# Performance work log

Measured on AMD Instinct MI355X. Metric: run time of the kernel, lower is better.

The kernel has to match this reference:

```python
import jax, jax.numpy as jnp
import numpy as np

EPS = 1e-8


def setup_inputs() -> dict:
    key = jax.random.key(0)
    k1, k2, k3 = jax.random.split(key, 3)
    B, N, M, C = 4, 4096, 16384, 256
    xyz = jax.random.normal(k1, (B * N, 3), dtype=jnp.float32)
    new_xyz = jax.random.normal(k2, (B * M, 3), dtype=jnp.float32)
    feat = jax.random.normal(k3, (B * N, C), dtype=jnp.float32)
    offset = jnp.arange(1, B + 1, dtype=jnp.int64) * N      # [4096, 8192, 12288, 16384]
    new_offset = jnp.arange(1, B + 1, dtype=jnp.int64) * M  # [16384, ..., 65536]
    return {"xyz": xyz, "new_xyz": new_xyz, "feat": feat,
            "offset": offset, "new_offset": new_offset, "k": 3}


def _interpolate(xyz_b, new_xyz_b, feat_b, k):
    # xyz_b: [B,N,3], new_xyz_b: [B,M,3], feat_b: [B,N,C]
    # pairwise squared distances via GEMM: [B,M,N]
    q2 = jnp.sum(new_xyz_b * new_xyz_b, axis=-1, keepdims=True)        # [B,M,1]
    s2 = jnp.sum(xyz_b * xyz_b, axis=-1)[:, None, :]                   # [B,1,N]
    cross = jnp.einsum('bmd,bnd->bmn', new_xyz_b, xyz_b)               # [B,M,N]
    d2 = q2 + s2 - 2.0 * cross                                         # [B,M,N]
    neg_d2, idx = jax.lax.top_k(-d2, k)                                # [B,M,k]
    dist = jnp.sqrt(jnp.maximum(-neg_d2, 1e-12))                       # euclidean, like knnquery
    dist_recip = 1.0 / (dist + EPS)
    weight = dist_recip / jnp.sum(dist_recip, axis=-1, keepdims=True)  # [B,M,k]
    gathered = jax.vmap(lambda f, i: f[i])(feat_b, idx)                # [B,M,k,C]
    return jnp.einsum('bmkc,bmk->bmc', gathered, weight)               # [B,M,C]


def reference(xyz, new_xyz, feat, offset, new_offset, k):
    B = offset.shape[0]
    N = xyz.shape[0] // B
    M = new_xyz.shape[0] // B
    C = feat.shape[1]
    # uniform offsets -> reshape into per-cloud batches
    out = _interpolate(xyz.reshape(B, N, 3), new_xyz.reshape(B, M, 3),
                       feat.reshape(B, N, C), k)
    return out.reshape(B * M, C)
```

## Files before the change

### kernel.cpp

```cpp
#include <hip/hip_runtime.h>
#include <float.h>


#define QPL   2
#define QPB   128
#define SPLIT 8
#define KEY_INIT 0x7FEFFFFFFFFFFFFFULL

#define NCA   16
#define NC    (NCA * NCA * NCA)
#define GMIN  (-4.0f)
#define HCELL (0.5f)
#define INVH  (2.0f)
#define SLACK (1e-3f)

typedef float v2f __attribute__((ext_vector_type(2)));

__device__ __forceinline__ double mk_key(float d2, int j) {
    unsigned long long u =
        ((unsigned long long)(unsigned)__float_as_uint(d2) << 32) | (unsigned)j;
    return __longlong_as_double(u);
}

__device__ __forceinline__ void ins3(double key, double& k0, double& k1,
                                     double& k2) {
    const double n0 = fmin(key, k0);
    const double n1 = fmin(fmax(key, k0), k1);
    const double n2 = fmin(fmax(key, k1), k2);
    k0 = n0; k1 = n1; k2 = n2;
}

__device__ __forceinline__ v2f dist2_pair(const v2f qx2, const v2f qy2,
                                          const v2f qz2, const v2f q22,
                                          const float4 p) {
    #pragma clang fp contract(off)
    const v2f px = {p.x, p.x};
    const v2f py = {p.y, p.y};
    const v2f pz = {p.z, p.z};
    const v2f pw = {p.w, p.w};
    const v2f t0 = qx2 * px;
    const v2f t1 = qy2 * py;
    const v2f t2 = t0 + t1;
    const v2f t3 = qz2 * pz;
    const v2f cr = t2 + t3;
    const v2f qs = q22 + pw;
    const v2f cc = cr + cr;
    const v2f d2 = qs - cc;
    return d2;
}

__device__ __forceinline__ float dist2_scalar(float qx, float qy, float qz,
                                              float q2, const float4 p) {
    #pragma clang fp contract(off)
    const float t0 = qx * p.x;
    const float t1 = qy * p.y;
    const float t2 = t0 + t1;
    const float t3 = qz * p.z;
    const float cr = t2 + t3;
    const float qs = q2 + p.w;
    const float cc = cr + cr;
    const float d2 = qs - cc;
    return d2;
}

__device__ __forceinline__ float sum_sq3(float x, float y, float z) {
    return __fadd_rn(__fadd_rn(__fmul_rn(x, x), __fmul_rn(y, y)),
                     __fmul_rn(z, z));
}

__device__ __forceinline__ int clampi(int v, int lo, int hi) {
    return v < lo ? lo : (v > hi ? hi : v);
}

__device__ __forceinline__ void cell3(float x, float y, float z,
                                      int& cx, int& cy, int& cz) {
    cx = clampi((int)floorf((x - GMIN) * INVH), 0, NCA - 1);
    cy = clampi((int)floorf((y - GMIN) * INVH), 0, NCA - 1);
    cz = clampi((int)floorf((z - GMIN) * INVH), 0, NCA - 1);
}

__global__ __launch_bounds__(1024) void grid_build(
    const float* __restrict__ xyz, const float* __restrict__ new_xyz,
    int* __restrict__ start, int* __restrict__ qstart,
    float4* __restrict__ spts, int* __restrict__ sidx,
    int* __restrict__ qsrt, int N, int M, int B)
{
    __shared__ int hist[NC];
    __shared__ int psum[1024];

    const int blk = blockIdx.x;
    const bool isQ = blk >= B;
    const int b = isQ ? blk - B : blk;
    const int nItems = isQ ? M : N;
    const float* __restrict__ src = isQ ? new_xyz + (size_t)b * M * 3
                                        : xyz + (size_t)b * N * 3;
    int* __restrict__ dst = isQ ? qstart : start;
    const int base = isQ ? b * M : b * N;
    const int t = threadIdx.x;

    #pragma unroll
    for (int c = t; c < NC; c += 1024) hist[c] = 0;
    __syncthreads();

    for (int i = t; i < nItems; i += 1024) {
        int cx, cy, cz;
        cell3(src[(size_t)i * 3 + 0], src[(size_t)i * 3 + 1],
              src[(size_t)i * 3 + 2], cx, cy, cz);
        atomicAdd(&hist[(cz * NCA + cy) * NCA + cx], 1);
    }
    __syncthreads();

    int loc0 = hist[t * 4 + 0], loc1 = hist[t * 4 + 1];
    int loc2 = hist[t * 4 + 2], loc3 = hist[t * 4 + 3];
    psum[t] = loc0 + loc1 + loc2 + loc3;
    __syncthreads();
    for (int off = 1; off < 1024; off <<= 1) {
        int v = 0;
        if (t >= off) v = psum[t - off];
        __syncthreads();
        psum[t] += v;
        __syncthreads();
    }
    int run = (t == 0 ? 0 : psum[t - 1]);
    dst[b * NC + t * 4 + 0] = base + run;  hist[t * 4 + 0] = run;  run += loc0;
    dst[b * NC + t * 4 + 1] = base + run;  hist[t * 4 + 1] = run;  run += loc1;
    dst[b * NC + t * 4 + 2] = base + run;  hist[t * 4 + 2] = run;  run += loc2;
    dst[b * NC + t * 4 + 3] = base + run;  hist[t * 4 + 3] = run;  run += loc3;
    if (!isQ && b == B - 1 && t == 1023) start[B * NC] = B * N;
    __syncthreads();

    for (int i = t; i < nItems; i += 1024) {
        const float x = src[(size_t)i * 3 + 0];
        const float y = src[(size_t)i * 3 + 1];
        const float z = src[(size_t)i * 3 + 2];
        int cx, cy, cz;
        cell3(x, y, z, cx, cy, cz);
        const int c = (cz * NCA + cy) * NCA + cx;
        const int slot = base + atomicAdd(&hist[c], 1);
        if (isQ) {
            qsrt[slot] = b * M + i;
        } else {
            spts[slot] = make_float4(x, y, z, sum_sq3(x, y, z));
            sidx[slot] = i;
        }
    }
}

__global__ __launch_bounds__(256, 8) void fp_knn_gather(
    const float* __restrict__ new_xyz,
    const float4* __restrict__ spts, const int* __restrict__ sidx,
    const int* __restrict__ start, const int* __restrict__ qsrt,
    const float4* __restrict__ feat4, float4* __restrict__ out4,
    int N, int M, int B) {
    __shared__ int   s_jb[16][3];
    __shared__ float s_wb[16][3];
    __shared__ int   s_qid[16];

    const int tid = threadIdx.x;
    const int grp = tid >> 4;
    const int s   = tid & 15;
    const int p   = blockIdx.x * 16 + grp;
    const int qid = qsrt[p];
    const int b   = qid / M;
    const int bNC = b * NC;

    const float qx = new_xyz[(size_t)qid * 3 + 0];
    const float qy = new_xyz[(size_t)qid * 3 + 1];
    const float qz = new_xyz[(size_t)qid * 3 + 2];
    const float q2 = sum_sq3(qx, qy, qz);

    int cx, cy, cz;
    cell3(qx, qy, qz, cx, cy, cz);

    const float bx0 = GMIN + (float)cx * HCELL;
    const float by0 = GMIN + (float)cy * HCELL;
    const float bz0 = GMIN + (float)cz * HCELL;
    const float ex = fmaxf(fmaxf(bx0 - qx, qx - (bx0 + HCELL)), 0.0f);
    const float ey = fmaxf(fmaxf(by0 - qy, qy - (by0 + HCELL)), 0.0f);
    const float ez = fmaxf(fmaxf(bz0 - qz, qz - (bz0 + HCELL)), 0.0f);
    const float e = fmaxf(ex, fmaxf(ey, ez));

    double k0 = __longlong_as_double(KEY_INIT), k1 = k0, k2 = k0;

    auto seg = [&](int x0, int x1, int cy2, int cz2) {
        const int rowbase = bNC + (cz2 * NCA + cy2) * NCA;
        const int j0 = start[rowbase + x0];
        const int j1 = start[rowbase + x1 + 1];
        for (int j = j0 + s; j < j1; j += 16) {
            const float4 pt = spts[j];
            const float d2 = dist2_scalar(qx, qy, qz, q2, pt);
            ins3(mk_key(d2, sidx[j]), k0, k1, k2);
        }
    };

    auto merge16 = [&](double& o0, double& o1, double& o2) {
        double t0 = k0, t1 = k1, t2 = k2;
        #pragma unroll
        for (int mask = 1; mask <= 8; mask <<= 1) {
            const double r0 = __shfl_xor(t0, mask, 16);
            const double r1 = __shfl_xor(t1, mask, 16);
            const double r2 = __shfl_xor(t2, mask, 16);
            ins3(r0, t0, t1, t2);
            ins3(r1, t0, t1, t2);
            ins3(r2, t0, t1, t2);
        }
        o0 = t0; o1 = t1; o2 = t2;
    };

    {
        const int z0 = clampi(cz - 1, 0, NCA - 1), z1 = clampi(cz + 1, 0, NCA - 1);
        const int y0 = clampi(cy - 1, 0, NCA - 1), y1 = clampi(cy + 1, 0, NCA - 1);
        const int x0 = clampi(cx - 1, 0, NCA - 1), x1 = clampi(cx + 1, 0, NCA - 1);
        for (int cz2 = z0; cz2 <= z1; ++cz2)
            for (int cy2 = y0; cy2 <= y1; ++cy2)
                seg(x0, x1, cy2, cz2);
    }

    for (int r = 2; r < NCA; ++r) {
        double m0, m1, m2;
        merge16(m0, m1, m2);
        const float d3 = __uint_as_float(
            (unsigned)((unsigned long long)__double_as_longlong(m2) >> 32));
        const float lb = fmaxf(HCELL * (float)(r - 1) - e, 0.0f);
        if (lb * lb > d3 + SLACK) break;
        const int z0 = clampi(cz - r, 0, NCA - 1), z1 = clampi(cz + r, 0, NCA - 1);
        const int y0 = clampi(cy - r, 0, NCA - 1), y1 = clampi(cy + r, 0, NCA - 1);
        const int x0 = clampi(cx - r, 0, NCA - 1), x1 = clampi(cx + r, 0, NCA - 1);
        for (int cz2 = z0; cz2 <= z1; ++cz2) {
            const int adz = cz2 >= cz ? cz2 - cz : cz - cz2;
            for (int cy2 = y0; cy2 <= y1; ++cy2) {
                const int ady = cy2 >= cy ? cy2 - cy : cy - cy2;
                if (adz == r || ady == r) {
                    seg(x0, x1, cy2, cz2);
                } else {
                    if (cx - r >= 0)       seg(cx - r, cx - r, cy2, cz2);
                    if (cx + r <= NCA - 1) seg(cx + r, cx + r, cy2, cz2);
                }
            }
        }
    }

    double f0, f1, f2;
    merge16(f0, f1, f2);
    if (s == 0) {
        const unsigned long long u0 = __double_as_longlong(f0);
        const unsigned long long u1 = __double_as_longlong(f1);
        const unsigned long long u2 = __double_as_longlong(f2);
        const float d0 = __uint_as_float((unsigned)(u0 >> 32));
        const float d1 = __uint_as_float((unsigned)(u1 >> 32));
        const float d2f = __uint_as_float((unsigned)(u2 >> 32));
        const float e0 = sqrtf(fmaxf(d0, 1e-12f));
        const float e1 = sqrtf(fmaxf(d1, 1e-12f));
        const float e2 = sqrtf(fmaxf(d2f, 1e-12f));
        const float r0 = 1.0f / (e0 + 1e-8f);
        const float r1 = 1.0f / (e1 + 1e-8f);
        const float r2 = 1.0f / (e2 + 1e-8f);
        const float rs = r0 + r1 + r2;
        s_jb[grp][0] = (int)(u0 & 0xffffffffu);
        s_jb[grp][1] = (int)(u1 & 0xffffffffu);
        s_jb[grp][2] = (int)(u2 & 0xffffffffu);
        s_wb[grp][0] = r0 / rs; s_wb[grp][1] = r1 / rs; s_wb[grp][2] = r2 / rs;
        s_qid[grp] = qid;
    }
    __syncthreads();

    const int lane = tid & 63;
    const int wv   = tid >> 6;
    #pragma unroll
    for (int t = 0; t < 4; ++t) {
        const int qq = wv * 4 + t;
        const int qid2 = s_qid[qq];
        const int b2 = qid2 / M;
        const int src_base = b2 * N;
        const int   a0 = s_jb[qq][0], a1 = s_jb[qq][1], a2 = s_jb[qq][2];
        const float u0 = s_wb[qq][0], u1 = s_wb[qq][1], u2 = s_wb[qq][2];
        const float4 f0v = feat4[(size_t)(src_base + a0) * 64 + lane];
        const float4 f1v = feat4[(size_t)(src_base + a1) * 64 + lane];
        const float4 f2v = feat4[(size_t)(src_base + a2) * 64 + lane];
        float4 o;
        o.x = u0 * f0v.x + u1 * f1v.x + u2 * f2v.x;
        o.y = u0 * f0v.y + u1 * f1v.y + u2 * f2v.y;
        o.z = u0 * f0v.z + u1 * f1v.z + u2 * f2v.z;
        o.w = u0 * f0v.w + u1 * f1v.w + u2 * f2v.w;
        out4[(size_t)qid2 * 64 + lane] = o;
    }
}

__global__ void pack_pts(const float* __restrict__ xyz,
                         float4* __restrict__ pts, int total) {
    int i = blockIdx.x * blockDim.x + threadIdx.x;
    if (i < total) {
        const float sx = xyz[(size_t)i * 3 + 0];
        const float sy = xyz[(size_t)i * 3 + 1];
        const float sz = xyz[(size_t)i * 3 + 2];
        pts[i] = make_float4(sx, sy, sz, sum_sq3(sx, sy, sz));
    }
}

template <int CHUNK>
__global__ __launch_bounds__(512, 4) void fp_knn_main(
    const float* __restrict__ new_xyz, const float4* __restrict__ pts,
    const float4* __restrict__ feat4, float4* __restrict__ out4,
    int N, int blocks_per_batch) {
    __shared__ double s_k[SPLIT][QPB][3];
    __shared__ float  s_w[QPB][3];
    __shared__ int    s_j[QPB][3];

    int g = blockIdx.x;
    if (gridDim.x == 512 && blocks_per_batch == 128) {
        const int xcd = g & 7, slot = g >> 3;
        g = (xcd >> 1) * 128 + (xcd & 1) * 64 + slot;
    }

    const int tid  = threadIdx.x;
    const int lane = tid & 63;
    const int b    = g / blocks_per_batch;
    const int src_base = b * N;
    const int m0 = g * QPB + lane;
    const int m1 = m0 + 64;

    const float q0x = new_xyz[(size_t)m0 * 3 + 0];
    const float q0y = new_xyz[(size_t)m0 * 3 + 1];
    const float q0z = new_xyz[(size_t)m0 * 3 + 2];
    const float q1x = new_xyz[(size_t)m1 * 3 + 0];
    const float q1y = new_xyz[(size_t)m1 * 3 + 1];
    const float q1z = new_xyz[(size_t)m1 * 3 + 2];
    const v2f qx2 = {q0x, q1x};
    const v2f qy2 = {q0y, q1y};
    const v2f qz2 = {q0z, q1z};
    const v2f q22 = {sum_sq3(q0x, q0y, q0z), sum_sq3(q1x, q1y, q1z)};

    const int cw    = tid >> 6;
    const int cbase = cw * CHUNK;
    const float4* __restrict__ cp = pts + src_base + cbase;

    double k00 = __longlong_as_double(KEY_INIT);
    double k01 = k00, k02 = k00;
    double k10 = k00, k11 = k00, k12 = k00;

    #pragma unroll 8
    for (int j = 0; j < CHUNK; ++j) {
        const float4 p = cp[j];
        const v2f d2 = dist2_pair(qx2, qy2, qz2, q22, p);
        ins3(mk_key(d2.x, cbase + j), k00, k01, k02);
        ins3(mk_key(d2.y, cbase + j), k10, k11, k12);
    }

    s_k[cw][lane][0]      = k00; s_k[cw][lane][1]      = k01; s_k[cw][lane][2]      = k02;
    s_k[cw][lane + 64][0] = k10; s_k[cw][lane + 64][1] = k11; s_k[cw][lane + 64][2] = k12;
    __syncthreads();

    if (tid < QPB) {
        double m0k = __longlong_as_double(KEY_INIT), m1k = m0k, m2k = m0k;
        #pragma unroll
        for (int ss = 0; ss < SPLIT; ++ss) {
            #pragma unroll
            for (int r = 0; r < 3; ++r) ins3(s_k[ss][tid][r], m0k, m1k, m2k);
        }
        unsigned long long u0 = __double_as_longlong(m0k);
        unsigned long long u1 = __double_as_longlong(m1k);
        unsigned long long u2 = __double_as_longlong(m2k);
        const float d0 = __uint_as_float((unsigned)(u0 >> 32));
        const float d1 = __uint_as_float((unsigned)(u1 >> 32));
        const float d2 = __uint_as_float((unsigned)(u2 >> 32));
        const float e0 = sqrtf(fmaxf(d0, 1e-12f));
        const float e1 = sqrtf(fmaxf(d1, 1e-12f));
        const float e2 = sqrtf(fmaxf(d2, 1e-12f));
        const float r0 = 1.0f / (e0 + 1e-8f);
        const float r1 = 1.0f / (e1 + 1e-8f);
        const float r2 = 1.0f / (e2 + 1e-8f);
        const float rs = r0 + r1 + r2;
        s_w[tid][0] = r0 / rs; s_w[tid][1] = r1 / rs; s_w[tid][2] = r2 / rs;
        s_j[tid][0] = (int)(u0 & 0xffffffffu);
        s_j[tid][1] = (int)(u1 & 0xffffffffu);
        s_j[tid][2] = (int)(u2 & 0xffffffffu);
    }
    __syncthreads();

    const int wv    = tid >> 6;
    const int qbase = g * QPB;
    #pragma unroll 4
    for (int t = 0; t < QPB / SPLIT; ++t) {
        const int qq = wv * (QPB / SPLIT) + t;
        const int   a0 = s_j[qq][0], a1 = s_j[qq][1], a2 = s_j[qq][2];
        const float u0 = s_w[qq][0], u1 = s_w[qq][1], u2 = s_w[qq][2];
        const float4 f0 = feat4[(size_t)(src_base + a0) * 64 + lane];
        const float4 f1 = feat4[(size_t)(src_base + a1) * 64 + lane];
        const float4 f2 = feat4[(size_t)(src_base + a2) * 64 + lane];
        float4 o;
        o.x = u0 * f0.x + u1 * f1.x + u2 * f2.x;
        o.y = u0 * f0.y + u1 * f1.y + u2 * f2.y;
        o.z = u0 * f0.z + u1 * f1.z + u2 * f2.z;
        o.w = u0 * f0.w + u1 * f1.w + u2 * f2.w;
        out4[(size_t)(qbase + qq) * 64 + lane] = o;
    }
}

__global__ void fp_knn_generic(
    const float* __restrict__ new_xyz, const float* __restrict__ xyz,
    const float* __restrict__ feat, float* __restrict__ out,
    int N, int M, int Btot) {
    const int m = blockIdx.x * blockDim.x + threadIdx.x;
    if (m >= Btot * M) return;
    const int b = m / M;
    const int src_base = b * N;
    const float qx = new_xyz[(size_t)m * 3 + 0];
    const float qy = new_xyz[(size_t)m * 3 + 1];
    const float qz = new_xyz[(size_t)m * 3 + 2];
    const float q2 = sum_sq3(qx, qy, qz);
    double k0 = __longlong_as_double(KEY_INIT), k1 = k0, k2 = k0;
    for (int j = 0; j < N; ++j) {
        const float sx = xyz[(size_t)(src_base + j) * 3 + 0];
        const float sy = xyz[(size_t)(src_base + j) * 3 + 1];
        const float sz = xyz[(size_t)(src_base + j) * 3 + 2];
        const float4 p = make_float4(sx, sy, sz, sum_sq3(sx, sy, sz));
        const float d2 = dist2_scalar(qx, qy, qz, q2, p);
        ins3(mk_key(d2, j), k0, k1, k2);
    }
    unsigned long long u0 = __double_as_longlong(k0);
    unsigned long long u1 = __double_as_longlong(k1);
    unsigned long long u2 = __double_as_longlong(k2);
    const float e0 = sqrtf(fmaxf(__uint_as_float((unsigned)(u0 >> 32)), 1e-12f));
    const float e1 = sqrtf(fmaxf(__uint_as_float((unsigned)(u1 >> 32)), 1e-12f));
    const float e2 = sqrtf(fmaxf(__uint_as_float((unsigned)(u2 >> 32)), 1e-12f));
    const float r0 = 1.0f / (e0 + 1e-8f);
    const float r1 = 1.0f / (e1 + 1e-8f);
    const float r2 = 1.0f / (e2 + 1e-8f);
    const float rs = r0 + r1 + r2;
    const float w0 = r0 / rs, w1 = r1 / rs, w2 = r2 / rs;
    const int a0 = (int)(u0 & 0xffffffffu), a1 = (int)(u1 & 0xffffffffu),
              a2 = (int)(u2 & 0xffffffffu);
    const int C = 256;
    for (int c = 0; c < C; ++c) {
        out[(size_t)m * C + c] =
            w0 * feat[(size_t)(src_base + a0) * C + c] +
            w1 * feat[(size_t)(src_base + a1) * C + c] +
            w2 * feat[(size_t)(src_base + a2) * C + c];
    }
}

extern "C" void kernel_launch(void* const* d_in, const int* in_sizes, int n_in,
                              void* d_out, int out_size, void* d_ws, size_t ws_size,
                              hipStream_t stream) {
    const float* xyz     = (const float*)d_in[0];
    const float* new_xyz = (const float*)d_in[1];
    const float* feat    = (const float*)d_in[2];
    float* out = (float*)d_out;

    const int B = in_sizes[3];
    const int N = in_sizes[0] / (3 * B);
    const int M = in_sizes[1] / (3 * B);
    const int Q = B * M;

    auto al = [](size_t x) { return (x + 255) & ~(size_t)255; };
    const size_t o_spts   = 0;
    const size_t o_sidx   = o_spts  + al((size_t)B * N * 16);
    const size_t o_start  = o_sidx  + al((size_t)B * N * 4);
    const size_t o_qstart = o_start + al(((size_t)B * NC + 1) * 4);
    const size_t o_qsort  = o_qstart+ al((size_t)B * NC * 4);
    const size_t need_grid = o_qsort + al((size_t)Q * 4);

    if ((Q % 16 == 0) && ws_size >= need_grid) {
        char* w = (char*)d_ws;
        float4* spts  = (float4*)(w + o_spts);
        int*   sidx   = (int*)  (w + o_sidx);
        int*   start  = (int*)  (w + o_start);
        int*   qstart = (int*)  (w + o_qstart);
        int*   qsrt   = (int*)  (w + o_qsort);

        grid_build<<<2 * B, 1024, 0, stream>>>(
            xyz, new_xyz, start, qstart, spts, sidx, qsrt, N, M, B);
        fp_knn_gather<<<Q / 16, 256, 0, stream>>>(
            new_xyz, spts, sidx, start, qsrt, (const float4*)feat,
            (float4*)out, N, M, B);
        return;
    }

    const size_t pts_bytes = (size_t)(B * N) * sizeof(float4);
    const bool fused_ok = (N % SPLIT == 0) && (N / SPLIT == 512) &&
                          (M % QPB == 0) && (ws_size >= pts_bytes);
    if (fused_ok) {
        pack_pts<<<(B * N + 255) / 256, 256, 0, stream>>>(xyz, (float4*)d_ws, B * N);
        const int blocks = Q / QPB;
        fp_knn_main<512><<<blocks, 512, 0, stream>>>(
            new_xyz, (const float4*)d_ws, (const float4*)feat, (float4*)out,
            N, M / QPB);
    } else {
        fp_knn_generic<<<(Q + 255) / 256, 256, 0, stream>>>(
            new_xyz, xyz, feat, out, N, M, B);
    }
}
```

Baseline: 199.7 us.

## Prune neighbor cells by box distance and gather per group without shared memory

The first ring of 26 neighbor cells is no longer scanned unconditionally. The kernel scans the query's own cell first, then visits each neighbor only if its box lower-bound distance is within the current group's third-nearest distance, refreshing that bound after each cell with a float-only shuffle merge. The final gather is done directly by each 16-lane group from registers, which removes the shared-memory staging and __syncthreads. The occupancy hint is also lowered. In exchange, there are more shuffle merges and per-cell start lookups, and the gather issues narrower 16-lane accesses per row.

```diff
diff --git a/kernel.cpp b/kernel.cpp
--- a/kernel.cpp
+++ b/kernel.cpp
@@ -28,6 +28,20 @@
     const double n1 = fmin(fmax(key, k0), k1);
     const double n2 = fmin(fmax(key, k1), k2);
     k0 = n0; k1 = n1; k2 = n2;
+}
+
+__device__ __forceinline__ void ins3f(float v, float& v0, float& v1,
+                                      float& v2) {
+    const float n0 = fminf(v, v0);
+    const float n1 = fminf(fmaxf(v, v0), v1);
+    const float n2 = fminf(fmaxf(v, v1), v2);
+    v0 = n0; v1 = n1; v2 = n2;
+}
+
+__device__ __forceinline__ float key_d2(double k) {
+    const unsigned long long u = __double_as_longlong(k);
+    const float v = __uint_as_float((unsigned)(u >> 32));
+    return (v == v) ? v : FLT_MAX;
 }
 
 __device__ __forceinline__ v2f dist2_pair(const v2f qx2, const v2f qy2,
@@ -146,16 +160,12 @@
     }
 }
 
-__global__ __launch_bounds__(256, 8) void fp_knn_gather(
+__global__ __launch_bounds__(256, 4) void fp_knn_gather(
     const float* __restrict__ new_xyz,
     const float4* __restrict__ spts, const int* __restrict__ sidx,
     const int* __restrict__ start, const int* __restrict__ qsrt,
     const float4* __restrict__ feat4, float4* __restrict__ out4,
     int N, int M, int B) {
-    __shared__ int   s_jb[16][3];
-    __shared__ float s_wb[16][3];
-    __shared__ int   s_qid[16];
-
     const int tid = threadIdx.x;
     const int grp = tid >> 4;
     const int s   = tid & 15;
@@ -175,6 +185,17 @@
     const float bx0 = GMIN + (float)cx * HCELL;
     const float by0 = GMIN + (float)cy * HCELL;
     const float bz0 = GMIN + (float)cz * HCELL;
+
+    const float dxm = fmaxf(0.0f, fmaxf((bx0 - HCELL) - qx, qx - bx0));
+    const float dxp = fmaxf(0.0f, fmaxf((bx0 + HCELL) - qx, qx - (bx0 + 2.0f * HCELL)));
+    const float dym = fmaxf(0.0f, fmaxf((by0 - HCELL) - qy, qy - by0));
+    const float dyp = fmaxf(0.0f, fmaxf((by0 + HCELL) - qy, qy - (by0 + 2.0f * HCELL)));
+    const float dzm = fmaxf(0.0f, fmaxf((bz0 - HCELL) - qz, qz - bz0));
+    const float dzp = fmaxf(0.0f, fmaxf((bz0 + HCELL) - qz, qz - (bz0 + 2.0f * HCELL)));
+    const float sqx[3] = {dxm * dxm, 0.0f, dxp * dxp};
+    const float sqy[3] = {dym * dym, 0.0f, dyp * dyp};
+    const float sqz[3] = {dzm * dzm, 0.0f, dzp * dzp};
+
     const float ex = fmaxf(fmaxf(bx0 - qx, qx - (bx0 + HCELL)), 0.0f);
     const float ey = fmaxf(fmaxf(by0 - qy, qy - (by0 + HCELL)), 0.0f);
     const float ez = fmaxf(fmaxf(bz0 - qz, qz - (bz0 + HCELL)), 0.0f);
@@ -182,7 +203,18 @@
 
     double k0 = __longlong_as_double(KEY_INIT), k1 = k0, k2 = k0;
 
-    auto seg = [&](int x0, int x1, int cy2, int cz2) {
+    auto scan_cell = [&](int cellIdx) {
+        const int gidx = bNC + cellIdx;
+        const int j0 = start[gidx];
+        const int j1 = start[gidx + 1];
+        for (int j = j0 + s; j < j1; j += 16) {
+            const float4 pt = spts[j];
+            const float d2 = dist2_scalar(qx, qy, qz, q2, pt);
+            ins3(mk_key(d2, sidx[j]), k0, k1, k2);
+        }
+    };
+
+    auto scan_span = [&](int x0, int x1, int cy2, int cz2) {
         const int rowbase = bNC + (cz2 * NCA + cy2) * NCA;
         const int j0 = start[rowbase + x0];
         const int j1 = start[rowbase + x1 + 1];
@@ -193,36 +225,47 @@
         }
     };
 
-    auto merge16 = [&](double& o0, double& o1, double& o2) {
-        double t0 = k0, t1 = k1, t2 = k2;
+    auto group_d3 = [&]() -> float {
+        float v0 = key_d2(k0), v1 = key_d2(k1), v2 = key_d2(k2);
         #pragma unroll
         for (int mask = 1; mask <= 8; mask <<= 1) {
-            const double r0 = __shfl_xor(t0, mask, 16);
-            const double r1 = __shfl_xor(t1, mask, 16);
-            const double r2 = __shfl_xor(t2, mask, 16);
-            ins3(r0, t0, t1, t2);
-            ins3(r1, t0, t1, t2);
-            ins3(r2, t0, t1, t2);
-        }
-        o0 = t0; o1 = t1; o2 = t2;
+            const float r0 = __shfl_xor(v0, mask, 16);
+            const float r1 = __shfl_xor(v1, mask, 16);
+            const float r2 = __shfl_xor(v2, mask, 16);
+            ins3f(r0, v0, v1, v2);
+            ins3f(r1, v0, v1, v2);
+            ins3f(r2, v0, v1, v2);
+        }
+        return v2;
     };
 
+    scan_cell((cz * NCA + cy) * NCA + cx);
+    float d3g = group_d3();
+
     {
-        const int z0 = clampi(cz - 1, 0, NCA - 1), z1 = clampi(cz + 1, 0, NCA - 1);
-        const int y0 = clampi(cy - 1, 0, NCA - 1), y1 = clampi(cy + 1, 0, NCA - 1);
-        const int x0 = clampi(cx - 1, 0, NCA - 1), x1 = clampi(cx + 1, 0, NCA - 1);
-        for (int cz2 = z0; cz2 <= z1; ++cz2)
-            for (int cy2 = y0; cy2 <= y1; ++cy2)
-                seg(x0, x1, cy2, cz2);
+        static constexpr int off[26][3] = {
+            {-1,0,0},{1,0,0},{0,-1,0},{0,1,0},{0,0,-1},{0,0,1},
+            {-1,-1,0},{-1,1,0},{1,-1,0},{1,1,0},
+            {-1,0,-1},{-1,0,1},{1,0,-1},{1,0,1},
+            {0,-1,-1},{0,-1,1},{0,1,-1},{0,1,1},
+            {-1,-1,-1},{-1,-1,1},{-1,1,-1},{-1,1,1},
+            {1,-1,-1},{1,-1,1},{1,1,-1},{1,1,1}};
+        #pragma unroll
+        for (int n = 0; n < 26; ++n) {
+            const int ox = off[n][0], oy = off[n][1], oz = off[n][2];
+            const int nx = cx + ox, ny = cy + oy, nz = cz + oz;
+            if (nx < 0 || nx >= NCA || ny < 0 || ny >= NCA ||
+                nz < 0 || nz >= NCA) continue;
+            const float db2 = sqx[ox + 1] + sqy[oy + 1] + sqz[oz + 1];
+            if (db2 > d3g + SLACK) continue;
+            scan_cell((nz * NCA + ny) * NCA + nx);
+            d3g = group_d3();
+        }
     }
 
     for (int r = 2; r < NCA; ++r) {
-        double m0, m1, m2;
-        merge16(m0, m1, m2);
-        const float d3 = __uint_as_float(
-            (unsigned)((unsigned long long)__double_as_longlong(m2) >> 32));
         const float lb = fmaxf(HCELL * (float)(r - 1) - e, 0.0f);
-        if (lb * lb > d3 + SLACK) break;
+        if (lb * lb > d3g + SLACK) break;
         const int z0 = clampi(cz - r, 0, NCA - 1), z1 = clampi(cz + r, 0, NCA - 1);
         const int y0 = clampi(cy - r, 0, NCA - 1), y1 = clampi(cy + r, 0, NCA - 1);
         const int x0 = clampi(cx - r, 0, NCA - 1), x1 = clampi(cx + r, 0, NCA - 1);
@@ -231,58 +274,62 @@
             for (int cy2 = y0; cy2 <= y1; ++cy2) {
                 const int ady = cy2 >= cy ? cy2 - cy : cy - cy2;
                 if (adz == r || ady == r) {
-                    seg(x0, x1, cy2, cz2);
+                    scan_span(x0, x1, cy2, cz2);
                 } else {
-                    if (cx - r >= 0)       seg(cx - r, cx - r, cy2, cz2);
-                    if (cx + r <= NCA - 1) seg(cx + r, cx + r, cy2, cz2);
+                    if (cx - r >= 0)       scan_span(cx - r, cx - r, cy2, cz2);
+                    if (cx + r <= NCA - 1) scan_span(cx + r, cx + r, cy2, cz2);
                 }
             }
         }
-    }
-
-    double f0, f1, f2;
-    merge16(f0, f1, f2);
-    if (s == 0) {
-        const unsigned long long u0 = __double_as_longlong(f0);
-        const unsigned long long u1 = __double_as_longlong(f1);
-        const unsigned long long u2 = __double_as_longlong(f2);
-        const float d0 = __uint_as_float((unsigned)(u0 >> 32));
-        const float d1 = __uint_as_float((unsigned)(u1 >> 32));
-        const float d2f = __uint_as_float((unsigned)(u2 >> 32));
-        const float e0 = sqrtf(fmaxf(d0, 1e-12f));
-        const float e1 = sqrtf(fmaxf(d1, 1e-12f));
-        const float e2 = sqrtf(fmaxf(d2f, 1e-12f));
-        const float r0 = 1.0f / (e0 + 1e-8f);
-        const float r1 = 1.0f / (e1 + 1e-8f);
-        const float r2 = 1.0f / (e2 + 1e-8f);
-        const float rs = r0 + r1 + r2;
-        s_jb[grp][0] = (int)(u0 & 0xffffffffu);
-        s_jb[grp][1] = (int)(u1 & 0xffffffffu);
-        s_jb[grp][2] = (int)(u2 & 0xffffffffu);
-        s_wb[grp][0] = r0 / rs; s_wb[grp][1] = r1 / rs; s_wb[grp][2] = r2 / rs;
-        s_qid[grp] = qid;
-    }
-    __syncthreads();
-
-    const int lane = tid & 63;
-    const int wv   = tid >> 6;
+        d3g = group_d3();
+    }
+
+    double f0 = k0, f1 = k1, f2 = k2;
+    #pragma unroll
+    for (int mask = 1; mask <= 8; mask <<= 1) {
+        const double r0 = __shfl_xor(f0, mask, 16);
+        const double r1 = __shfl_xor(f1, mask, 16);
+        const double r2 = __shfl_xor(f2, mask, 16);
+        ins3(r0, f0, f1, f2);
+        ins3(r1, f0, f1, f2);
+        ins3(r2, f0, f1, f2);
+    }
+
+    const unsigned long long u0 = __double_as_longlong(f0);
+    const unsigned long long u1 = __double_as_longlong(f1);
+    const unsigned long long u2 = __double_as_longlong(f2);
+    const float d0 = __uint_as_float((unsigned)(u0 >> 32));
+    const float d1 = __uint_as_float((unsigned)(u1 >> 32));
+    const float d2f = __uint_as_float((unsigned)(u2 >> 32));
+    const float e0 = sqrtf(fmaxf(d0, 1e-12f));
+    const float e1 = sqrtf(fmaxf(d1, 1e-12f));
+    const float e2 = sqrtf(fmaxf(d2f, 1e-12f));
+    const float r0 = 1.0f / (e0 + 1e-8f);
+    const float r1 = 1.0f / (e1 + 1e-8f);
+    const float r2 = 1.0f / (e2 + 1e-8f);
+    const float rs = r0 + r1 + r2;
+    const float u0w = r0 / rs, u1w = r1 / rs, u2w = r2 / rs;
+    const int a0 = (int)(u0 & 0xffffffffu);
+    const int a1 = (int)(u1 & 0xffffffffu);
+    const int a2 = (int)(u2 & 0xffffffffu);
+
+    const int src_base = b * N;
+    const size_t r0b = (size_t)(src_base + a0) * 64;
+    const size_t r1b = (size_t)(src_base + a1) * 64;
+    const size_t r2b = (size_t)(src_base + a2) * 64;
+    const size_t ob  = (size_t)qid * 64;
     #pragma unroll
     for (int t = 0; t < 4; ++t) {
-        const int qq = wv * 4 + t;
-        const int qid2 = s_qid[qq];
-        const int b2 = qid2 / M;
-        const int src_base = b2 * N;
-        const int   a0 = s_jb[qq][0], a1 = s_jb[qq][1], a2 = s_jb[qq][2];
-        const float u0 = s_wb[qq][0], u1 = s_wb[qq][1], u2 = s_wb[qq][2];
-        const float4 f0v = feat4[(size_t)(src_base + a0) * 64 + lane];
-        const float4 f1v = feat4[(size_t)(src_base + a1) * 64 + lane];
-        const float4 f2v = feat4[(size_t)(src_base + a2) * 64 + lane];
+        const int c = s + t * 16;
+        const float4 f0v = feat4[r0b + c];
+        const float4 f1v = feat4[r1b + c];
+        const float4 f2v = feat4[r2b + c];
         float4 o;
-        o.x = u0 * f0v.x + u1 * f1v.x + u2 * f2v.x;
-        o.y = u0 * f0v.y + u1 * f1v.y + u2 * f2v.y;
-        o.z = u0 * f0v.z + u1 * f1v.z + u2 * f2v.z;
-        o.w = u0 * f0v.w + u1 * f1v.w + u2 * f2v.w;
-        out4[(size_t)qid2 * 64 + lane] = o;
+        o.x = u0w * f0v.x + u1w * f1v.x + u2w * f2v.x;
+        o.y = u0w * f0v.y + u1w * f1v.y + u2w * f2v.y;
+        o.z = u0w * f0v.z + u1w * f1v.z + u2w * f2v.z;
+        o.w = u0w * f0v.w + u1w * f1v.w + u2w * f2v.w;
+        out4[ob + c] = o;
     }
 }
 
```

New measurement: 218.8 us. 9.6% more time.
